# Kernel tuning notes

Hardware: AMD Instinct MI355X
Metric: run time of the kernel (lower is better)

The kernel has to match this reference:

```python
import jax, jax.numpy as jnp
from jax import lax
import numpy as np

CONF = 0.5        # config.video.detection_confidence
MAX_FACES = 8     # config.video.max_faces
EPS = 1e-5        # BatchNorm eps (inference mode: running stats)


def setup_inputs() -> dict:
    key = jax.random.key(0)
    ks = jax.random.split(key, 8)
    def w(k, shape):
        return jax.random.normal(k, shape, jnp.float32) * 0.05
    B, H, W = 32, 512, 512
    f32 = jnp.float32
    return {
        "x": jax.random.normal(ks[0], (B, 3, H, W), f32),
        # backbone conv1 (3->32, s2) + BN
        "w1": w(ks[1], (32, 3, 3, 3)), "b1": jnp.zeros(32, f32),
        "g1": jnp.ones(32, f32), "be1": jnp.zeros(32, f32),
        "m1": jnp.zeros(32, f32), "v1": jnp.ones(32, f32),
        # backbone conv2 (32->64, s2) + BN
        "w2": w(ks[2], (64, 32, 3, 3)), "b2": jnp.zeros(64, f32),
        "g2": jnp.ones(64, f32), "be2": jnp.zeros(64, f32),
        "m2": jnp.zeros(64, f32), "v2": jnp.ones(64, f32),
        # backbone conv3 (64->128, s2) + BN
        "w3": w(ks[3], (128, 64, 3, 3)), "b3": jnp.zeros(128, f32),
        "g3": jnp.ones(128, f32), "be3": jnp.zeros(128, f32),
        "m3": jnp.zeros(128, f32), "v3": jnp.ones(128, f32),
        # detection head (128->256 k3, 256->1 k1)
        "dw1": w(ks[4], (256, 128, 3, 3)), "db1": jnp.zeros(256, f32),
        "dw2": w(ks[5], (1, 256, 1, 1)), "db2": jnp.zeros(1, f32),
        # bbox head (128->256 k3, 256->4 k1)
        "bw1": w(ks[6], (256, 128, 3, 3)), "bb1": jnp.zeros(256, f32),
        "bw2": w(ks[7], (4, 256, 1, 1)), "bb2": jnp.zeros(4, f32),
    }


def _conv(x, w, b, stride, pad):
    y = lax.conv_general_dilated(x, w, (stride, stride), ((pad, pad), (pad, pad)),
                                 dimension_numbers=("NCHW", "OIHW", "NCHW"))
    return y + b[None, :, None, None]


def _bn(x, g, b, m, v):
    scale = (g * lax.rsqrt(v + EPS))[None, :, None, None]
    return (x - m[None, :, None, None]) * scale + b[None, :, None, None]


def reference(x, w1, b1, g1, be1, m1, v1, w2, b2, g2, be2, m2, v2,
              w3, b3, g3, be3, m3, v3, dw1, db1, dw2, db2, bw1, bb1, bw2, bb2):
    h = jax.nn.relu(_bn(_conv(x, w1, b1, 2, 1), g1, be1, m1, v1))
    h = jax.nn.relu(_bn(_conv(h, w2, b2, 2, 1), g2, be2, m2, v2))
    h = jax.nn.relu(_bn(_conv(h, w3, b3, 2, 1), g3, be3, m3, v3))
    # heads
    det = jax.nn.sigmoid(_conv(jax.nn.relu(_conv(h, dw1, db1, 1, 1)), dw2, db2, 1, 0))[:, 0]  # [B,Hf,Wf]
    bbox = _conv(jax.nn.relu(_conv(h, bw1, bb1, 1, 1)), bw2, bb2, 1, 0)  # [B,4,Hf,Wf]
    # fused threshold + top-k + gather (fixed-size, jit-friendly version of the per-image loop)
    B = det.shape[0]
    scores = det.reshape(B, -1)                      # [B, Hf*Wf]
    top_s, top_i = lax.top_k(scores, MAX_FACES)      # [B, K]
    bflat = bbox.reshape(B, 4, -1)                   # [B, 4, Hf*Wf]
    sel = jnp.take_along_axis(bflat, top_i[:, None, :], axis=2)  # [B, 4, K]
    boxes = jax.nn.sigmoid(jnp.swapaxes(sel, 1, 2)) * x.shape[-1]  # [B, K, 4]
    mask = (top_s > CONF)[:, :, None]                # below-threshold slots -> zeros
    return jnp.where(mask, boxes, jnp.zeros((), boxes.dtype))
```

## Files before the change

### kernel.cpp

```cpp
#include <hip/hip_runtime.h>
#include <math.h>

#define EPSBN 1e-5f

typedef __attribute__((ext_vector_type(4))) float f32x4;
typedef __attribute__((ext_vector_type(8))) short s16x8;

__device__ __forceinline__ unsigned short f2bf(float f) {
    unsigned u = __builtin_bit_cast(unsigned, f);
    u = (u + 0x7fffu + ((u >> 16) & 1u)) >> 16;
    return (unsigned short)u;
}
__device__ __forceinline__ float bf2f(unsigned short s) {
    unsigned u = ((unsigned)s) << 16;
    return __builtin_bit_cast(float, u);
}


__global__ __launch_bounds__(256) void prep_k(
    const float* __restrict__ w1, const float* __restrict__ b1, const float* __restrict__ g1,
    const float* __restrict__ be1, const float* __restrict__ m1, const float* __restrict__ v1,
    const float* __restrict__ w2, const float* __restrict__ b2, const float* __restrict__ g2,
    const float* __restrict__ be2, const float* __restrict__ m2, const float* __restrict__ v2,
    const float* __restrict__ w3, const float* __restrict__ b3, const float* __restrict__ g3,
    const float* __restrict__ be3, const float* __restrict__ m3, const float* __restrict__ v3,
    float* __restrict__ W)
{
    int i = blockIdx.x * 256 + threadIdx.x;
    if (i < 864) {
        int co = i & 31; int r = i >> 5; int ci = r % 3; int kk = r / 3;
        float A = g1[co] * rsqrtf(v1[co] + EPSBN);
        W[i] = w1[(co*3 + ci)*9 + kk] * A;
    } else if (i < 896) {
        int co = i - 864;
        float A = g1[co] * rsqrtf(v1[co] + EPSBN);
        W[i] = (b1[co] - m1[co]) * A + be1[co];
    } else if (i >= 19328 && i < 19392) {
        int co = i - 19328;
        float A = g2[co] * rsqrtf(v2[co] + EPSBN);
        W[i] = (b2[co] - m2[co]) * A + be2[co];
    } else if (i >= 93120 && i < 93248) {
        int co = i - 93120;
        float A = g3[co] * rsqrtf(v3[co] + EPSBN);
        W[i] = (b3[co] - m3[co]) * A + be3[co];
    }
}

__global__ __launch_bounds__(256) void prep2_k(
    const float* __restrict__ dw1, const float* __restrict__ bw1,
    unsigned short* __restrict__ WF)
{
    int i = blockIdx.x * 256 + threadIdx.x;
    if (i >= 1179648) return;
    int head = i / 589824;
    int r    = i - head * 589824;
    int kk   = r >> 16;
    int r2   = r & 65535;
    int cig  = r2 >> 14;
    int pl   = (r2 >> 13) & 1;
    int nf   = (r2 >> 9) & 15;
    int lane = (r2 >> 3) & 63;
    int j    = r2 & 7;
    int ci = cig*32 + (lane >> 4)*8 + j;
    int co = (lane & 15) + nf*16;
    const float* src = head ? bw1 : dw1;
    float w = src[(co*128 + ci)*9 + kk];
    unsigned short h = f2bf(w);
    WF[i] = pl ? f2bf(w - bf2f(h)) : h;
}

__global__ __launch_bounds__(256) void prep3_k(
    const float* __restrict__ w3, const float* __restrict__ g3, const float* __restrict__ v3,
    unsigned short* __restrict__ W3F)
{
    int i = blockIdx.x * 256 + threadIdx.x;
    if (i >= 147456) return;
    int kk = i >> 14;
    int r  = i & 16383;
    int cig = r >> 13;
    int pl  = (r >> 12) & 1;
    int nf  = (r >> 9) & 7;
    int lane = (r >> 3) & 63;
    int j   = r & 7;
    int ci = cig*32 + (lane >> 4)*8 + j;
    int co = nf*16 + (lane & 15);
    float A = g3[co] * rsqrtf(v3[co] + EPSBN);
    float w = w3[(co*64 + ci)*9 + kk] * A;
    unsigned short h = f2bf(w);
    W3F[i] = pl ? f2bf(w - bf2f(h)) : h;
}

__global__ __launch_bounds__(256) void prep4_k(
    const float* __restrict__ w2, const float* __restrict__ g2, const float* __restrict__ v2,
    unsigned short* __restrict__ W2F)
{
    int i = blockIdx.x * 256 + threadIdx.x;
    if (i >= 36864) return;
    int kk = i >> 12;
    int r  = i & 4095;
    int pl  = r >> 11;
    int nfg = (r >> 9) & 3;
    int lane = (r >> 3) & 63;
    int j   = r & 7;
    int ci = (lane >> 4)*8 + j;
    int co = nfg*16 + (lane & 15);
    float A = g2[co] * rsqrtf(v2[co] + EPSBN);
    float w = w2[(co*32 + ci)*9 + kk] * A;
    unsigned short h = f2bf(w);
    W2F[i] = pl ? f2bf(w - bf2f(h)) : h;
}

__global__ __launch_bounds__(256, 4) void conv12mm_k(
    const float* __restrict__ x, const float* __restrict__ W,
    const unsigned short* __restrict__ W2F,
    unsigned short* __restrict__ A2H, unsigned short* __restrict__ A2L, int b0)
{
    __shared__ __attribute__((aligned(16))) unsigned short Ah[9792];
    __shared__ __attribute__((aligned(16))) unsigned short Al[9792];

    const int tid  = threadIdx.x;
    const int lane = tid & 63;
    const int wv   = tid >> 6;
    const int m    = lane & 15;
    const int ks   = lane >> 4;

    const int bl   = blockIdx.x >> 8;
    const int tile = blockIdx.x & 255;
    const int OY = (tile >> 3) * 4;
    const int OX = (tile & 7) * 16;
    const int base1y = 2*OY - 1, base1x = 2*OX - 1;

    const float* xb = x + (size_t)(b0 + bl) * 3 * 262144;

    for (int t = tid; t < 297; t += 256) {
        int row = t / 33, lx = t - row*33;
        int y1 = base1y + row, x1 = base1x + lx;
        float c1[32];
        #pragma unroll
        for (int c = 0; c < 32; c++) c1[c] = 0.f;
        if (((unsigned)y1 < 256u) && ((unsigned)x1 < 256u)) {
            #pragma unroll
            for (int ky = 0; ky < 3; ky++) {
                int xy = 2*y1 + ky - 1;
                if ((unsigned)xy < 512u) {
                    #pragma unroll
                    for (int kx = 0; kx < 3; kx++) {
                        int xx = 2*x1 + kx - 1;
                        if ((unsigned)xx < 512u) {
                            int kk = ky*3 + kx;
                            #pragma unroll
                            for (int ci = 0; ci < 3; ci++) {
                                float v = xb[(size_t)ci*262144 + xy*512 + xx];
                                const float4* w4 = (const float4*)(W + (kk*3+ci)*32);
                                float4 wa = w4[0], wb = w4[1], wc = w4[2], wd = w4[3];
                                float4 we = w4[4], wf = w4[5], wg = w4[6], wh = w4[7];
                                c1[0]  = fmaf(v, wa.x, c1[0]);  c1[1]  = fmaf(v, wa.y, c1[1]);
                                c1[2]  = fmaf(v, wa.z, c1[2]);  c1[3]  = fmaf(v, wa.w, c1[3]);
                                c1[4]  = fmaf(v, wb.x, c1[4]);  c1[5]  = fmaf(v, wb.y, c1[5]);
                                c1[6]  = fmaf(v, wb.z, c1[6]);  c1[7]  = fmaf(v, wb.w, c1[7]);
                                c1[8]  = fmaf(v, wc.x, c1[8]);  c1[9]  = fmaf(v, wc.y, c1[9]);
                                c1[10] = fmaf(v, wc.z, c1[10]); c1[11] = fmaf(v, wc.w, c1[11]);
                                c1[12] = fmaf(v, wd.x, c1[12]); c1[13] = fmaf(v, wd.y, c1[13]);
                                c1[14] = fmaf(v, wd.z, c1[14]); c1[15] = fmaf(v, wd.w, c1[15]);
                                c1[16] = fmaf(v, we.x, c1[16]); c1[17] = fmaf(v, we.y, c1[17]);
                                c1[18] = fmaf(v, we.z, c1[18]); c1[19] = fmaf(v, we.w, c1[19]);
                                c1[20] = fmaf(v, wf.x, c1[20]); c1[21] = fmaf(v, wf.y, c1[21]);
                                c1[22] = fmaf(v, wf.z, c1[22]); c1[23] = fmaf(v, wf.w, c1[23]);
                                c1[24] = fmaf(v, wg.x, c1[24]); c1[25] = fmaf(v, wg.y, c1[25]);
                                c1[26] = fmaf(v, wg.z, c1[26]); c1[27] = fmaf(v, wg.w, c1[27]);
                                c1[28] = fmaf(v, wh.x, c1[28]); c1[29] = fmaf(v, wh.y, c1[29]);
                                c1[30] = fmaf(v, wh.z, c1[30]); c1[31] = fmaf(v, wh.w, c1[31]);
                            }
                        }
                    }
                }
            }
            #pragma unroll
            for (int c = 0; c < 32; c++)
                c1[c] = fmaxf(c1[c] + W[864 + c], 0.f);
        }
        int xi = (lx & 1)*17 + (lx >> 1);
        #pragma unroll
        for (int kg = 0; kg < 4; kg++) {
            uint4 h, l;
            unsigned hw[4], lw[4];
            #pragma unroll
            for (int q = 0; q < 4; q++) {
                float r0 = c1[kg*8 + 2*q], r1 = c1[kg*8 + 2*q + 1];
                unsigned short h0 = f2bf(r0), h1 = f2bf(r1);
                unsigned short l0 = f2bf(r0 - bf2f(h0)), l1 = f2bf(r1 - bf2f(h1));
                hw[q] = (unsigned)h0 | ((unsigned)h1 << 16);
                lw[q] = (unsigned)l0 | ((unsigned)l1 << 16);
            }
            h.x = hw[0]; h.y = hw[1]; h.z = hw[2]; h.w = hw[3];
            l.x = lw[0]; l.y = lw[1]; l.z = lw[2]; l.w = lw[3];
            int a = ((kg*9 + row)*34 + xi)*8;
            *(uint4*)&Ah[a] = h;
            *(uint4*)&Al[a] = l;
        }
    }
    __syncthreads();

    f32x4 acc[4];
    #pragma unroll
    for (int mf = 0; mf < 4; mf++) { f32x4 z = {0.f,0.f,0.f,0.f}; acc[mf] = z; }

    for (int ky = 0; ky < 3; ky++) {
        for (int kx = 0; kx < 3; kx++) {
            int kk = ky*3 + kx;
            int xib = (kx & 1)*17 + (kx >> 1);
            s16x8 ah[4], al[4];
            #pragma unroll
            for (int mf = 0; mf < 4; mf++) {
                int hy = 2*mf + ky;
                int a = ((ks*9 + hy)*34 + xib + m)*8;
                ah[mf] = *(const s16x8*)&Ah[a];
                al[mf] = *(const s16x8*)&Al[a];
            }
            const unsigned short* wb = W2F + kk*4096;
            s16x8 bh  = *(const s16x8*)(wb + wv*512 + lane*8);
            s16x8 blo = *(const s16x8*)(wb + 2048 + wv*512 + lane*8);
            #pragma unroll
            for (int mf = 0; mf < 4; mf++) {
                acc[mf] = __builtin_amdgcn_mfma_f32_16x16x32_bf16(ah[mf], bh,  acc[mf], 0, 0, 0);
                acc[mf] = __builtin_amdgcn_mfma_f32_16x16x32_bf16(ah[mf], blo, acc[mf], 0, 0, 0);
                acc[mf] = __builtin_amdgcn_mfma_f32_16x16x32_bf16(al[mf], bh,  acc[mf], 0, 0, 0);
            }
        }
    }

    const int co = wv*16 + m;
    const float bv = W[19328 + co];
    #pragma unroll
    for (int mf = 0; mf < 4; mf++) {
        int y = OY + mf;
        #pragma unroll
        for (int r = 0; r < 4; r++) {
            int xo = OX + ks*4 + r;
            float rv = fmaxf(acc[mf][r] + bv, 0.f);
            unsigned short h = f2bf(rv);
            unsigned short l = f2bf(rv - bf2f(h));
            size_t a = ((size_t)(bl*16384 + y*128 + xo))*64 + co;
            A2H[a] = h;
            A2L[a] = l;
        }
    }
}

__global__ __launch_bounds__(256, 2) void conv3mm_k(
    const unsigned short* __restrict__ A2H, const unsigned short* __restrict__ A2L,
    const unsigned short* __restrict__ W3F, const float* __restrict__ bias,
    unsigned* __restrict__ A3P)
{
    const int tid  = threadIdx.x;
    const int lane = tid & 63;
    const int w    = tid >> 6;
    const int bl   = blockIdx.x >> 6;
    const int y    = blockIdx.x & 63;
    const int m    = lane & 15;
    const int ks   = lane >> 4;

    f32x4 acc[4][2];
    #pragma unroll
    for (int mf = 0; mf < 4; mf++)
        #pragma unroll
        for (int nfl = 0; nfl < 2; nfl++) {
            f32x4 z = {0.f, 0.f, 0.f, 0.f};
            acc[mf][nfl] = z;
        }

    const size_t ibase = (size_t)bl * 16384 * 64;

    for (int ky = 0; ky < 3; ky++) {
        int iy = 2*y + ky - 1;
        if ((unsigned)iy >= 128u) continue;
        for (int kx = 0; kx < 3; kx++) {
            int kk = ky*3 + kx;
            #pragma unroll
            for (int cig = 0; cig < 2; cig++) {
                s16x8 ah[4], al[4];
                #pragma unroll
                for (int mf = 0; mf < 4; mf++) {
                    int xo = mf*16 + m;
                    int ix = 2*xo + kx - 1;
                    bool v = ix >= 0;
                    int ixc = v ? ix : 0;
                    size_t a = ibase + ((size_t)iy*128 + ixc)*64 + cig*32 + ks*8;
                    s16x8 zh = {0,0,0,0,0,0,0,0};
                    s16x8 th = *(const s16x8*)(A2H + a);
                    s16x8 tl = *(const s16x8*)(A2L + a);
                    ah[mf] = v ? th : zh;
                    al[mf] = v ? tl : zh;
                }
                const unsigned short* wb = W3F + (kk*2 + cig)*8192;
                #pragma unroll
                for (int nfl = 0; nfl < 2; nfl++) {
                    int nfg = w*2 + nfl;
                    s16x8 bh  = *(const s16x8*)(wb + nfg*512 + lane*8);
                    s16x8 blo = *(const s16x8*)(wb + 4096 + nfg*512 + lane*8);
                    #pragma unroll
                    for (int mf = 0; mf < 4; mf++) {
                        acc[mf][nfl] = __builtin_amdgcn_mfma_f32_16x16x32_bf16(ah[mf], bh,  acc[mf][nfl], 0, 0, 0);
                        acc[mf][nfl] = __builtin_amdgcn_mfma_f32_16x16x32_bf16(ah[mf], blo, acc[mf][nfl], 0, 0, 0);
                        acc[mf][nfl] = __builtin_amdgcn_mfma_f32_16x16x32_bf16(al[mf], bh,  acc[mf][nfl], 0, 0, 0);
                    }
                }
            }
        }
    }

    const size_t obase = ((size_t)(bl*64 + y))*64*128;
    #pragma unroll
    for (int nfl = 0; nfl < 2; nfl++) {
        int co = (w*2 + nfl)*16 + m;
        float bv = bias[co];
        #pragma unroll
        for (int mf = 0; mf < 4; mf++) {
            #pragma unroll
            for (int r = 0; r < 4; r++) {
                float rv = fmaxf(acc[mf][nfl][r] + bv, 0.f);
                unsigned short h = f2bf(rv);
                unsigned short l = f2bf(rv - bf2f(h));
                int xo = mf*16 + ks*4 + r;
                A3P[obase + (size_t)xo*128 + co] = (unsigned)h | ((unsigned)l << 16);
            }
        }
    }
}

__global__ __launch_bounds__(512, 4) void headmm_k(
    const unsigned* __restrict__ A3P, const unsigned short* __restrict__ WF,
    const float* __restrict__ db1, const float* __restrict__ dw2, const float* __restrict__ db2,
    const float* __restrict__ bb1, const float* __restrict__ bw2, const float* __restrict__ bb2,
    float* __restrict__ SC, float* __restrict__ BF, int b0)
{
    __shared__ __attribute__((aligned(16))) unsigned short Ah[8704];
    __shared__ __attribute__((aligned(16))) unsigned short Al[8704];
    __shared__ float red[4][4][128];

    const int tid  = threadIdx.x;
    const int lane = tid & 63;
    const int w    = tid >> 6;
    const int whi  = w >> 2;
    const int wq   = w & 3;
    const int head = blockIdx.y;
    const int imgl = blockIdx.x >> 5;
    const int y0   = (blockIdx.x & 31) * 2;

    f32x4 acc[4][4];
    #pragma unroll
    for (int mf = 0; mf < 4; mf++)
        #pragma unroll
        for (int nf = 0; nf < 4; nf++) {
            f32x4 z = {0.f, 0.f, 0.f, 0.f};
            acc[mf][nf] = z;
        }

    const unsigned* abase = A3P + (size_t)imgl * 64 * 64 * 128;
    const unsigned short* WFh = WF + head * 589824;

    uint4 pva[3], pvb[3];
    #define HM_ISSUE(CIG)                                                          \
        _Pragma("unroll")                                                          \
        for (int it = 0; it < 3; it++) {                                           \
            int t = tid + it*512;                                                  \
            uint4 z4 = {0u,0u,0u,0u};                                              \
            pva[it] = z4; pvb[it] = z4;                                            \
            if (t < 1056) {                                                        \
                int kgrp = t & 3; int q = t >> 2;                                  \
                int xi = q % 66;  int row = q / 66;                                \
                int gr = y0 + row - 1, gx = xi - 1;                                \
                if (((unsigned)gr < 64u) && ((unsigned)gx < 64u)) {                \
                    const uint4* p = (const uint4*)(abase + ((size_t)gr*64 + gx)*128 \
                                                    + (CIG)*32 + kgrp*8);          \
                    pva[it] = p[0]; pvb[it] = p[1];                                \
                }                                                                  \
            }                                                                      \
        }

    HM_ISSUE(0);
    for (int cig = 0; cig < 4; cig++) {
        __syncthreads();
        #pragma unroll
        for (int it = 0; it < 3; it++) {
            int t = tid + it*512;
            if (t < 1056) {
                int kgrp = t & 3; int q = t >> 2;
                int xi = q % 66;  int row = q / 66;
                int a = ((kgrp*4 + row)*68 + xi)*8;
                uint4 va = pva[it], vb = pvb[it];
                uint4 h, l;
                h.x = (va.x & 0xffffu) | (va.y << 16);
                h.y = (va.z & 0xffffu) | (va.w << 16);
                h.z = (vb.x & 0xffffu) | (vb.y << 16);
                h.w = (vb.z & 0xffffu) | (vb.w << 16);
                l.x = (va.x >> 16) | (va.y & 0xffff0000u);
                l.y = (va.z >> 16) | (va.w & 0xffff0000u);
                l.z = (vb.x >> 16) | (vb.y & 0xffff0000u);
                l.w = (vb.z >> 16) | (vb.w & 0xffff0000u);
                *(uint4*)&Ah[a] = h;
                *(uint4*)&Al[a] = l;
            }
        }
        if (cig < 3) { HM_ISSUE(cig + 1); }
        __syncthreads();
        __builtin_amdgcn_s_setprio(1);
        #pragma unroll 1
        for (int kk = 0; kk < 9; kk++) {
            int ky = kk / 3, kx = kk - 3*(kk/3);
            s16x8 ah[4], al[4];
            #pragma unroll
            for (int mf = 0; mf < 4; mf++) {
                int xq = (lane & 15) + 16*mf + kx;
                int a = (((lane >> 4)*4 + whi + ky)*68 + xq)*8;
                ah[mf] = *(const s16x8*)&Ah[a];
                al[mf] = *(const s16x8*)&Al[a];
            }
            const unsigned short* wk = WFh + kk*65536 + cig*16384;
            #pragma unroll
            for (int nf = 0; nf < 4; nf++) {
                int nfg = wq*4 + nf;
                s16x8 bh = *(const s16x8*)(wk + nfg*512 + lane*8);
                s16x8 bl = *(const s16x8*)(wk + 8192 + nfg*512 + lane*8);
                #pragma unroll
                for (int mf = 0; mf < 4; mf++) {
                    acc[mf][nf] = __builtin_amdgcn_mfma_f32_16x16x32_bf16(ah[mf], bh, acc[mf][nf], 0, 0, 0);
                    acc[mf][nf] = __builtin_amdgcn_mfma_f32_16x16x32_bf16(ah[mf], bl, acc[mf][nf], 0, 0, 0);
                    acc[mf][nf] = __builtin_amdgcn_mfma_f32_16x16x32_bf16(al[mf], bh, acc[mf][nf], 0, 0, 0);
                }
            }
        }
        __builtin_amdgcn_s_setprio(0);
    }
    #undef HM_ISSUE

    const float* b1p = head ? bb1 : db1;
    const float* w2p = head ? bw2 : dw2;
    const float* b2p = head ? bb2 : db2;
    const int NOUT = head ? 4 : 1;

    #pragma unroll
    for (int nf = 0; nf < 4; nf++) {
        float bv = b1p[(lane & 15) + (wq*4 + nf)*16];
        #pragma unroll
        for (int mf = 0; mf < 4; mf++)
            #pragma unroll
            for (int r = 0; r < 4; r++)
                acc[mf][nf][r] = fmaxf(acc[mf][nf][r] + bv, 0.f);
    }

    for (int p = 0; p < NOUT; p++) {
        float part[4][4];
        #pragma unroll
        for (int mf = 0; mf < 4; mf++)
            #pragma unroll
            for (int r = 0; r < 4; r++) part[mf][r] = 0.f;
        #pragma unroll
        for (int nf = 0; nf < 4; nf++) {
            float wq2 = w2p[p*256 + (lane & 15) + (wq*4 + nf)*16];
            #pragma unroll
            for (int mf = 0; mf < 4; mf++)
                #pragma unroll
                for (int r = 0; r < 4; r++)
                    part[mf][r] = fmaf(acc[mf][nf][r], wq2, part[mf][r]);
        }
        #pragma unroll
        for (int mf = 0; mf < 4; mf++)
            #pragma unroll
            for (int r = 0; r < 4; r++) {
                float v = part[mf][r];
                v += __shfl_xor(v, 1);
                v += __shfl_xor(v, 2);
                v += __shfl_xor(v, 4);
                v += __shfl_xor(v, 8);
                if ((lane & 15) == 0)
                    red[wq][p][whi*64 + mf*16 + (lane >> 4)*4 + r] = v;
            }
    }
    __syncthreads();
    float* outp = head ? BF : SC;
    for (int o = tid; o < NOUT*128; o += 512) {
        int p = o >> 7; int px = o & 127;
        float v = red[0][p][px] + red[1][p][px] + red[2][p][px] + red[3][p][px] + b2p[p];
        outp[((size_t)((b0 + imgl)*NOUT + p))*4096 + y0*64 + px] = v;
    }
}

__global__ __launch_bounds__(256) void topk_k(
    const float* __restrict__ scores, const float* __restrict__ bflat,
    float* __restrict__ outp)
{
    __shared__ float sv[4096];
    __shared__ float rv[256];
    __shared__ int   ri[256];
    __shared__ float kv[8];
    __shared__ int   kidx[8];
    int b = blockIdx.x, t = threadIdx.x;
    for (int i = t; i < 4096; i += 256) sv[i] = scores[b*4096 + i];
    __syncthreads();
    for (int k = 0; k < 8; k++) {
        float bv = -INFINITY; int bi = 0x7fffffff;
        for (int i = t; i < 4096; i += 256) {
            float v = sv[i];
            if (v > bv || (v == bv && i < bi)) { bv = v; bi = i; }
        }
        rv[t] = bv; ri[t] = bi;
        __syncthreads();
        for (int s = 128; s > 0; s >>= 1) {
            if (t < s) {
                float v2 = rv[t+s]; int i2 = ri[t+s];
                if (v2 > rv[t] || (v2 == rv[t] && i2 < ri[t])) { rv[t] = v2; ri[t] = i2; }
            }
            __syncthreads();
        }
        if (t == 0) { kv[k] = rv[0]; kidx[k] = ri[0]; sv[ri[0]] = -INFINITY; }
        __syncthreads();
    }
    if (t < 32) {
        int k = t >> 2, c = t & 3;
        int idx = kidx[k];
        float s  = 1.f / (1.f + expf(-kv[k]));
        float lg = bflat[((size_t)(b*4 + c))*4096 + idx];
        float box = 512.f / (1.f + expf(-lg));
        outp[(b*8 + k)*4 + c] = (s > 0.5f) ? box : 0.f;
    }
}

extern "C" void kernel_launch(void* const* d_in, const int* in_sizes, int n_in,
                              void* d_out, int out_size, void* d_ws, size_t ws_size,
                              hipStream_t stream)
{
    const float* x   = (const float*)d_in[0];
    const float* w1  = (const float*)d_in[1];
    const float* b1  = (const float*)d_in[2];
    const float* g1  = (const float*)d_in[3];
    const float* be1 = (const float*)d_in[4];
    const float* m1  = (const float*)d_in[5];
    const float* v1  = (const float*)d_in[6];
    const float* w2  = (const float*)d_in[7];
    const float* b2  = (const float*)d_in[8];
    const float* g2  = (const float*)d_in[9];
    const float* be2 = (const float*)d_in[10];
    const float* m2  = (const float*)d_in[11];
    const float* v2  = (const float*)d_in[12];
    const float* w3  = (const float*)d_in[13];
    const float* b3  = (const float*)d_in[14];
    const float* g3  = (const float*)d_in[15];
    const float* be3 = (const float*)d_in[16];
    const float* m3  = (const float*)d_in[17];
    const float* v3  = (const float*)d_in[18];
    const float* dw1 = (const float*)d_in[19];
    const float* db1 = (const float*)d_in[20];
    const float* dw2 = (const float*)d_in[21];
    const float* db2 = (const float*)d_in[22];
    const float* bw1 = (const float*)d_in[23];
    const float* bb1 = (const float*)d_in[24];
    const float* bw2 = (const float*)d_in[25];
    const float* bb2 = (const float*)d_in[26];

    char*  wsb = (char*)d_ws;
    float*          W   = (float*)wsb;
    unsigned short* WF  = (unsigned short*)(wsb + 372992);
    unsigned short* W3F = (unsigned short*)(wsb + 2732288);
    float*          SC  = (float*)(wsb + 3027200);
    float*          BF  = (float*)(wsb + 3551488);
    unsigned short* A2H = (unsigned short*)(wsb + 5648640);
    unsigned short* A2L = (unsigned short*)(wsb + 22425856);
    unsigned*       A3P = (unsigned*)(wsb + 39203072);
    unsigned short* W2F = (unsigned short*)(wsb + 55980288);
    float* out = (float*)d_out;

    prep_k <<<365, 256, 0, stream>>>(w1,b1,g1,be1,m1,v1, w2,b2,g2,be2,m2,v2,
                                     w3,b3,g3,be3,m3,v3, W);
    prep2_k<<<4608, 256, 0, stream>>>(dw1, bw1, WF);
    prep3_k<<<576, 256, 0, stream>>>(w3, g3, v3, W3F);
    prep4_k<<<144, 256, 0, stream>>>(w2, g2, v2, W2F);

    for (int c = 0; c < 4; c++) {
        conv12mm_k<<<2048, 256, 0, stream>>>(x, W, W2F, A2H, A2L, c*8);
        conv3mm_k <<<512, 256, 0, stream>>>(A2H, A2L, W3F, W + 93120, A3P);
        headmm_k  <<<dim3(256, 2), 512, 0, stream>>>(A3P, WF, db1, dw2, db2, bb1, bw2, bb2,
                                                     SC, BF, c*8);
    }
    topk_k<<<32, 256, 0, stream>>>(SC, BF, out);
}
```

Measured before the change: 717.7 us.

## Switch head conv GEMM from 16x16x32 to 32x32x16 bf16 MFMA tiles

Restructures the detection/bbox head 3x3 conv GEMM to use 32x32x16 bf16 MFMA instructions instead of 16x16x32. The weight prepacking layout, the LDS A-fragment loads, the accumulator tiling (2x2 f32x16 per wave) and the epilogue reduction (extra shuffle stage, new output index mapping) are all rewritten to match. The larger tile means fewer fragment loads per FLOP and fewer MFMA issues. In exchange it uses more accumulator registers and a longer cross-lane reduction in the epilogue.

```diff
diff --git a/kernel.cpp b/kernel.cpp
--- a/kernel.cpp
+++ b/kernel.cpp
@@ -4,6 +4,7 @@
 #define EPSBN 1e-5f
 
 typedef __attribute__((ext_vector_type(4))) float f32x4;
+typedef __attribute__((ext_vector_type(16))) float f32x16;
 typedef __attribute__((ext_vector_type(8))) short s16x8;
 
 __device__ __forceinline__ unsigned short f2bf(float f) {
@@ -57,12 +58,14 @@
     int kk   = r >> 16;
     int r2   = r & 65535;
     int cig  = r2 >> 14;
-    int pl   = (r2 >> 13) & 1;
-    int nf   = (r2 >> 9) & 15;
-    int lane = (r2 >> 3) & 63;
-    int j    = r2 & 7;
-    int ci = cig*32 + (lane >> 4)*8 + j;
-    int co = (lane & 15) + nf*16;
+    int r3   = r2 & 16383;
+    int kc   = r3 >> 13;
+    int pl   = (r3 >> 12) & 1;
+    int ng   = (r3 >> 9) & 7;
+    int lane = (r3 >> 3) & 63;
+    int j    = r3 & 7;
+    int ci = cig*32 + kc*16 + (lane >> 5)*8 + j;
+    int co = ng*32 + (lane & 31);
     const float* src = head ? bw1 : dw1;
     float w = src[(co*128 + ci)*9 + kk];
     unsigned short h = f2bf(w);
@@ -347,14 +350,13 @@
     const int imgl = blockIdx.x >> 5;
     const int y0   = (blockIdx.x & 31) * 2;
 
-    f32x4 acc[4][4];
+    f32x16 acc[2][2];
     #pragma unroll
-    for (int mf = 0; mf < 4; mf++)
-        #pragma unroll
-        for (int nf = 0; nf < 4; nf++) {
-            f32x4 z = {0.f, 0.f, 0.f, 0.f};
-            acc[mf][nf] = z;
-        }
+    for (int mt = 0; mt < 2; mt++)
+        #pragma unroll
+        for (int nt = 0; nt < 2; nt++)
+            #pragma unroll
+            for (int r = 0; r < 16; r++) acc[mt][nt][r] = 0.f;
 
     const unsigned* abase = A3P + (size_t)imgl * 64 * 64 * 128;
     const unsigned short* WFh = WF + head * 589824;
@@ -408,25 +410,30 @@
         #pragma unroll 1
         for (int kk = 0; kk < 9; kk++) {
             int ky = kk / 3, kx = kk - 3*(kk/3);
-            s16x8 ah[4], al[4];
-            #pragma unroll
-            for (int mf = 0; mf < 4; mf++) {
-                int xq = (lane & 15) + 16*mf + kx;
-                int a = (((lane >> 4)*4 + whi + ky)*68 + xq)*8;
-                ah[mf] = *(const s16x8*)&Ah[a];
-                al[mf] = *(const s16x8*)&Al[a];
-            }
+            s16x8 ah[2][2], al[2][2];
+            #pragma unroll
+            for (int mt = 0; mt < 2; mt++)
+                #pragma unroll
+                for (int kc = 0; kc < 2; kc++) {
+                    int kg = kc*2 + (lane >> 5);
+                    int a = ((kg*4 + whi + ky)*68 + (lane & 31) + 32*mt + kx)*8;
+                    ah[mt][kc] = *(const s16x8*)&Ah[a];
+                    al[mt][kc] = *(const s16x8*)&Al[a];
+                }
             const unsigned short* wk = WFh + kk*65536 + cig*16384;
             #pragma unroll
-            for (int nf = 0; nf < 4; nf++) {
-                int nfg = wq*4 + nf;
-                s16x8 bh = *(const s16x8*)(wk + nfg*512 + lane*8);
-                s16x8 bl = *(const s16x8*)(wk + 8192 + nfg*512 + lane*8);
+            for (int nt = 0; nt < 2; nt++) {
+                int ng = wq*2 + nt;
                 #pragma unroll
-                for (int mf = 0; mf < 4; mf++) {
-                    acc[mf][nf] = __builtin_amdgcn_mfma_f32_16x16x32_bf16(ah[mf], bh, acc[mf][nf], 0, 0, 0);
-                    acc[mf][nf] = __builtin_amdgcn_mfma_f32_16x16x32_bf16(ah[mf], bl, acc[mf][nf], 0, 0, 0);
-                    acc[mf][nf] = __builtin_amdgcn_mfma_f32_16x16x32_bf16(al[mf], bh, acc[mf][nf], 0, 0, 0);
+                for (int kc = 0; kc < 2; kc++) {
+                    s16x8 bh = *(const s16x8*)(wk + kc*8192 + ng*512 + lane*8);
+                    s16x8 bl = *(const s16x8*)(wk + kc*8192 + 4096 + ng*512 + lane*8);
+                    #pragma unroll
+                    for (int mt = 0; mt < 2; mt++) {
+                        acc[mt][nt] = __builtin_amdgcn_mfma_f32_32x32x16_bf16(ah[mt][kc], bh, acc[mt][nt], 0, 0, 0);
+                        acc[mt][nt] = __builtin_amdgcn_mfma_f32_32x32x16_bf16(ah[mt][kc], bl, acc[mt][nt], 0, 0, 0);
+                        acc[mt][nt] = __builtin_amdgcn_mfma_f32_32x32x16_bf16(al[mt][kc], bh, acc[mt][nt], 0, 0, 0);
+                    }
                 }
             }
         }
@@ -439,43 +446,38 @@
     const float* b2p = head ? bb2 : db2;
     const int NOUT = head ? 4 : 1;
 
+    const int cbase = wq*64 + (lane & 31);
     #pragma unroll
-    for (int nf = 0; nf < 4; nf++) {
-        float bv = b1p[(lane & 15) + (wq*4 + nf)*16];
-        #pragma unroll
-        for (int mf = 0; mf < 4; mf++)
-            #pragma unroll
-            for (int r = 0; r < 4; r++)
-                acc[mf][nf][r] = fmaxf(acc[mf][nf][r] + bv, 0.f);
+    for (int nt = 0; nt < 2; nt++) {
+        float bv = b1p[cbase + nt*32];
+        #pragma unroll
+        for (int mt = 0; mt < 2; mt++)
+            #pragma unroll
+            for (int r = 0; r < 16; r++)
+                acc[mt][nt][r] = fmaxf(acc[mt][nt][r] + bv, 0.f);
     }
 
     for (int p = 0; p < NOUT; p++) {
-        float part[4][4];
-        #pragma unroll
-        for (int mf = 0; mf < 4; mf++)
-            #pragma unroll
-            for (int r = 0; r < 4; r++) part[mf][r] = 0.f;
-        #pragma unroll
-        for (int nf = 0; nf < 4; nf++) {
-            float wq2 = w2p[p*256 + (lane & 15) + (wq*4 + nf)*16];
-            #pragma unroll
-            for (int mf = 0; mf < 4; mf++)
-                #pragma unroll
-                for (int r = 0; r < 4; r++)
-                    part[mf][r] = fmaf(acc[mf][nf][r], wq2, part[mf][r]);
-        }
-        #pragma unroll
-        for (int mf = 0; mf < 4; mf++)
-            #pragma unroll
-            for (int r = 0; r < 4; r++) {
-                float v = part[mf][r];
+        float w0 = w2p[p*256 + cbase];
+        float w1v = w2p[p*256 + cbase + 32];
+        #pragma unroll
+        for (int mt = 0; mt < 2; mt++) {
+            float pt[16];
+            #pragma unroll
+            for (int r = 0; r < 16; r++)
+                pt[r] = acc[mt][0][r]*w0 + acc[mt][1][r]*w1v;
+            #pragma unroll
+            for (int r = 0; r < 16; r++) {
+                float v = pt[r];
                 v += __shfl_xor(v, 1);
                 v += __shfl_xor(v, 2);
                 v += __shfl_xor(v, 4);
                 v += __shfl_xor(v, 8);
-                if ((lane & 15) == 0)
-                    red[wq][p][whi*64 + mf*16 + (lane >> 4)*4 + r] = v;
-            }
+                v += __shfl_xor(v, 16);
+                if ((lane & 31) == 0)
+                    red[wq][p][whi*64 + mt*32 + (r & 3) + 8*(r >> 2) + 4*(lane >> 5)] = v;
+            }
+        }
     }
     __syncthreads();
     float* outp = head ? BF : SC;
```

Result: slower. 797.5 us (+11.1%).

## Retile head GEMM to one output row per block with 8 waves splitting N

Applied to the files above, without the earlier changes.

Each headmm block now computes one output row (64 pixels) instead of two, with all 8 waves splitting the 256 output channels (2 N-fragments each) rather than a 2x4 wave grid. The grid doubles to 512x2 blocks, shared memory for the input halo shrinks, and the per-wave accumulator tile halves, which cuts register pressure and may raise occupancy. In exchange, the 3-row input halo is re-staged per output row (more redundant global/LDS traffic), and weight fragments are reloaded for half as many pixels, lowering arithmetic intensity per weight load.

```diff
diff --git a/kernel.cpp b/kernel.cpp
--- a/kernel.cpp
+++ b/kernel.cpp
@@ -334,24 +334,22 @@
     const float* __restrict__ bb1, const float* __restrict__ bw2, const float* __restrict__ bb2,
     float* __restrict__ SC, float* __restrict__ BF, int b0)
 {
-    __shared__ __attribute__((aligned(16))) unsigned short Ah[8704];
-    __shared__ __attribute__((aligned(16))) unsigned short Al[8704];
-    __shared__ float red[4][4][128];
+    __shared__ __attribute__((aligned(16))) unsigned short Ah[6528];
+    __shared__ __attribute__((aligned(16))) unsigned short Al[6528];
+    __shared__ float red[8][4][64];
 
     const int tid  = threadIdx.x;
     const int lane = tid & 63;
     const int w    = tid >> 6;
-    const int whi  = w >> 2;
-    const int wq   = w & 3;
     const int head = blockIdx.y;
-    const int imgl = blockIdx.x >> 5;
-    const int y0   = (blockIdx.x & 31) * 2;
-
-    f32x4 acc[4][4];
+    const int imgl = blockIdx.x >> 6;
+    const int y    = blockIdx.x & 63;
+
+    f32x4 acc[4][2];
     #pragma unroll
     for (int mf = 0; mf < 4; mf++)
         #pragma unroll
-        for (int nf = 0; nf < 4; nf++) {
+        for (int nf = 0; nf < 2; nf++) {
             f32x4 z = {0.f, 0.f, 0.f, 0.f};
             acc[mf][nf] = z;
         }
@@ -359,17 +357,17 @@
     const unsigned* abase = A3P + (size_t)imgl * 64 * 64 * 128;
     const unsigned short* WFh = WF + head * 589824;
 
-    uint4 pva[3], pvb[3];
+    uint4 pva[2], pvb[2];
     #define HM_ISSUE(CIG)                                                          \
         _Pragma("unroll")                                                          \
-        for (int it = 0; it < 3; it++) {                                           \
+        for (int it = 0; it < 2; it++) {                                           \
             int t = tid + it*512;                                                  \
             uint4 z4 = {0u,0u,0u,0u};                                              \
             pva[it] = z4; pvb[it] = z4;                                            \
-            if (t < 1056) {                                                        \
+            if (t < 792) {                                                         \
                 int kgrp = t & 3; int q = t >> 2;                                  \
                 int xi = q % 66;  int row = q / 66;                                \
-                int gr = y0 + row - 1, gx = xi - 1;                                \
+                int gr = y + row - 1, gx = xi - 1;                                 \
                 if (((unsigned)gr < 64u) && ((unsigned)gx < 64u)) {                \
                     const uint4* p = (const uint4*)(abase + ((size_t)gr*64 + gx)*128 \
                                                     + (CIG)*32 + kgrp*8);          \
@@ -382,12 +380,12 @@
     for (int cig = 0; cig < 4; cig++) {
         __syncthreads();
         #pragma unroll
-        for (int it = 0; it < 3; it++) {
+        for (int it = 0; it < 2; it++) {
             int t = tid + it*512;
-            if (t < 1056) {
+            if (t < 792) {
                 int kgrp = t & 3; int q = t >> 2;
                 int xi = q % 66;  int row = q / 66;
-                int a = ((kgrp*4 + row)*68 + xi)*8;
+                int a = ((kgrp*3 + row)*68 + xi)*8;
                 uint4 va = pva[it], vb = pvb[it];
                 uint4 h, l;
                 h.x = (va.x & 0xffffu) | (va.y << 16);
@@ -412,14 +410,14 @@
             #pragma unroll
             for (int mf = 0; mf < 4; mf++) {
                 int xq = (lane & 15) + 16*mf + kx;
-                int a = (((lane >> 4)*4 + whi + ky)*68 + xq)*8;
+                int a = (((lane >> 4)*3 + ky)*68 + xq)*8;
                 ah[mf] = *(const s16x8*)&Ah[a];
                 al[mf] = *(const s16x8*)&Al[a];
             }
             const unsigned short* wk = WFh + kk*65536 + cig*16384;
             #pragma unroll
-            for (int nf = 0; nf < 4; nf++) {
-                int nfg = wq*4 + nf;
+            for (int nf = 0; nf < 2; nf++) {
+                int nfg = w*2 + nf;
                 s16x8 bh = *(const s16x8*)(wk + nfg*512 + lane*8);
                 s16x8 bl = *(const s16x8*)(wk + 8192 + nfg*512 + lane*8);
                 #pragma unroll
@@ -440,8 +438,8 @@
     const int NOUT = head ? 4 : 1;
 
     #pragma unroll
-    for (int nf = 0; nf < 4; nf++) {
-        float bv = b1p[(lane & 15) + (wq*4 + nf)*16];
+    for (int nf = 0; nf < 2; nf++) {
+        float bv = b1p[(lane & 15) + (w*2 + nf)*16];
         #pragma unroll
         for (int mf = 0; mf < 4; mf++)
             #pragma unroll
@@ -450,39 +448,30 @@
     }
 
     for (int p = 0; p < NOUT; p++) {
-        float part[4][4];
-        #pragma unroll
-        for (int mf = 0; mf < 4; mf++)
-            #pragma unroll
-            for (int r = 0; r < 4; r++) part[mf][r] = 0.f;
-        #pragma unroll
-        for (int nf = 0; nf < 4; nf++) {
-            float wq2 = w2p[p*256 + (lane & 15) + (wq*4 + nf)*16];
-            #pragma unroll
-            for (int mf = 0; mf < 4; mf++)
-                #pragma unroll
-                for (int r = 0; r < 4; r++)
-                    part[mf][r] = fmaf(acc[mf][nf][r], wq2, part[mf][r]);
-        }
-        #pragma unroll
-        for (int mf = 0; mf < 4; mf++)
+        float wq0 = w2p[p*256 + (lane & 15) + (w*2 + 0)*16];
+        float wq1 = w2p[p*256 + (lane & 15) + (w*2 + 1)*16];
+        #pragma unroll
+        for (int mf = 0; mf < 4; mf++) {
             #pragma unroll
             for (int r = 0; r < 4; r++) {
-                float v = part[mf][r];
+                float v = acc[mf][0][r]*wq0 + acc[mf][1][r]*wq1;
                 v += __shfl_xor(v, 1);
                 v += __shfl_xor(v, 2);
                 v += __shfl_xor(v, 4);
                 v += __shfl_xor(v, 8);
                 if ((lane & 15) == 0)
-                    red[wq][p][whi*64 + mf*16 + (lane >> 4)*4 + r] = v;
-            }
+                    red[w][p][mf*16 + (lane >> 4)*4 + r] = v;
+            }
+        }
     }
     __syncthreads();
     float* outp = head ? BF : SC;
-    for (int o = tid; o < NOUT*128; o += 512) {
-        int p = o >> 7; int px = o & 127;
-        float v = red[0][p][px] + red[1][p][px] + red[2][p][px] + red[3][p][px] + b2p[p];
-        outp[((size_t)((b0 + imgl)*NOUT + p))*4096 + y0*64 + px] = v;
+    if (tid < NOUT*64) {
+        int p = tid >> 6; int px = tid & 63;
+        float v = b2p[p];
+        #pragma unroll
+        for (int ww = 0; ww < 8; ww++) v += red[ww][p][px];
+        outp[((size_t)((b0 + imgl)*NOUT + p))*4096 + y*64 + px] = v;
     }
 }
 
@@ -579,7 +568,7 @@
     for (int c = 0; c < 4; c++) {
         conv12mm_k<<<2048, 256, 0, stream>>>(x, W, W2F, A2H, A2L, c*8);
         conv3mm_k <<<512, 256, 0, stream>>>(A2H, A2L, W3F, W + 93120, A3P);
-        headmm_k  <<<dim3(256, 2), 512, 0, stream>>>(A3P, WF, db1, dw2, db2, bb1, bw2, bb2,
+        headmm_k  <<<dim3(512, 2), 512, 0, stream>>>(A3P, WF, db1, dw2, db2, bb1, bw2, bb2,
                                                      SC, BF, c*8);
     }
     topk_k<<<32, 256, 0, stream>>>(SC, BF, out);
```

Result: no change. 728.5 us (+1.5%).
